# Kernel optimization log

Measured on AMD Instinct MI355X. Metric: run time of the kernel, lower is better.

## Reference

```python
import jax, jax.numpy as jnp
import numpy as np

PARTITION_LENGTH = 64
NUM_PARTITIONS = 1024
BATCH = 2048


def setup_inputs() -> dict:
    key = jax.random.key(0)
    x = jax.random.normal(key, (BATCH, NUM_PARTITIONS * PARTITION_LENGTH), dtype=jnp.float32)
    return {"x": x}


def reference(x) -> jnp.ndarray:
    # Each nn.Linear(partition_length, 1, bias=False) has weight fixed to ones,
    # so it is a sum over a contiguous partition of the feature dim.
    B = x.shape[0]
    # [B, P*L] -> [B, P, L] -> sum over L -> [B, P]
    return x.reshape(B, NUM_PARTITIONS, PARTITION_LENGTH).sum(axis=-1)
```

## Files before the change

### kernel.cpp

```cpp
#include <hip/hip_runtime.h>
#include <hip/hip_bf16.h>


__global__ __launch_bounds__(256) void PartialSum_85478439125876_kernel(
    const float4* __restrict__ x4, float* __restrict__ out, long long n4) {
    long long tid = (long long)blockIdx.x * blockDim.x + threadIdx.x;
    if (tid >= n4) return;

    float4 v = x4[tid];
    float s = v.x + v.y + v.z + v.w;

    s += __shfl_xor(s, 1, 64);
    s += __shfl_xor(s, 2, 64);
    s += __shfl_xor(s, 4, 64);
    s += __shfl_xor(s, 8, 64);

    if ((threadIdx.x & 15) == 0) {
        out[tid >> 4] = s;
    }
}

extern "C" void kernel_launch(void* const* d_in, const int* in_sizes, int n_in,
                              void* d_out, int out_size, void* d_ws, size_t ws_size,
                              hipStream_t stream) {
    const float* x = (const float*)d_in[0];
    float* out = (float*)d_out;

    long long n = (long long)in_sizes[0];
    long long n4 = n / 4;

    const int BLOCK = 256;
    long long grid = (n4 + BLOCK - 1) / BLOCK;

    PartialSum_85478439125876_kernel<<<(unsigned)grid, BLOCK, 0, stream>>>(
        (const float4*)x, out, n4);
}
```

Measured before the change: 651.7 us.

## Stage input via direct global-to-LDS loads and sum partitions per thread

Each block now pulls 64KB of input straight into LDS with global_load_lds 16-byte async loads, then each thread sums one 64-float partition from LDS using swizzled float4 reads. This removes the per-thread cross-lane shuffle reduction and the 1-in-16 output writes, giving coalesced one-output-per-thread stores. In exchange it uses 64KB of LDS per block, which caps occupancy, and the bounds check is gone, so it assumes the input size divides evenly into blocks.

```diff
diff --git a/kernel.cpp b/kernel.cpp
--- a/kernel.cpp
+++ b/kernel.cpp
@@ -1,23 +1,59 @@
 #include <hip/hip_runtime.h>
 #include <hip/hip_bf16.h>
+#include <stdint.h>
 
 
-__global__ __launch_bounds__(256) void PartialSum_85478439125876_kernel(
-    const float4* __restrict__ x4, float* __restrict__ out, long long n4) {
-    long long tid = (long long)blockIdx.x * blockDim.x + threadIdx.x;
-    if (tid >= n4) return;
+#define BLOCK 256
+#define F4_PER_BLOCK 4096
 
-    float4 v = x4[tid];
-    float s = v.x + v.y + v.z + v.w;
+typedef const __attribute__((address_space(1))) uint32_t glb_u32;
+typedef __attribute__((address_space(3))) uint32_t lds_u32;
 
-    s += __shfl_xor(s, 1, 64);
-    s += __shfl_xor(s, 2, 64);
-    s += __shfl_xor(s, 4, 64);
-    s += __shfl_xor(s, 8, 64);
+__global__ __launch_bounds__(BLOCK, 2) void PartialSum_85478439125876_kernel(
+    const float* __restrict__ x, float* __restrict__ out) {
+    __shared__ float4 smem[F4_PER_BLOCK];
 
-    if ((threadIdx.x & 15) == 0) {
-        out[tid >> 4] = s;
+    const int tid = threadIdx.x;
+    const int wave = tid >> 6;
+    const int lane = tid & 63;
+
+    const float* gbase = x + (size_t)blockIdx.x * (F4_PER_BLOCK * 4);
+
+#pragma unroll
+    for (int t = 0; t < 16; ++t) {
+        const int f4 = t * 256 + wave * 64 + lane;
+        glb_u32* g = (glb_u32*)(gbase + (size_t)f4 * 4);
+        lds_u32* l = (lds_u32*)(smem + (t * 256 + wave * 64));
+        __builtin_amdgcn_global_load_lds(g, l, 16, 0, 0);
     }
+
+    __syncthreads();
+
+    const float4* s4 = (const float4*)smem;
+    const int base = tid * 16;
+    const int sw = tid & 7;
+
+    float4 a0 = s4[base + (0 ^ sw)];
+    float4 a1 = s4[base + (1 ^ sw)];
+    float4 a2 = s4[base + (2 ^ sw)];
+    float4 a3 = s4[base + (3 ^ sw)];
+#pragma unroll
+    for (int q = 4; q < 16; q += 4) {
+        float4 v0 = s4[base + ((q + 0) ^ sw)];
+        float4 v1 = s4[base + ((q + 1) ^ sw)];
+        float4 v2 = s4[base + ((q + 2) ^ sw)];
+        float4 v3 = s4[base + ((q + 3) ^ sw)];
+        a0.x += v0.x; a0.y += v0.y; a0.z += v0.z; a0.w += v0.w;
+        a1.x += v1.x; a1.y += v1.y; a1.z += v1.z; a1.w += v1.w;
+        a2.x += v2.x; a2.y += v2.y; a2.z += v2.z; a2.w += v2.w;
+        a3.x += v3.x; a3.y += v3.y; a3.z += v3.z; a3.w += v3.w;
+    }
+    a0.x += a1.x; a0.y += a1.y; a0.z += a1.z; a0.w += a1.w;
+    a2.x += a3.x; a2.y += a3.y; a2.z += a3.z; a2.w += a3.w;
+    a0.x += a2.x; a0.y += a2.y; a0.z += a2.z; a0.w += a2.w;
+    float s = (a0.x + a0.y) + (a0.z + a0.w);
+
+    out[(size_t)blockIdx.x * BLOCK + tid] = s;
 }
 
 extern "C" void kernel_launch(void* const* d_in, const int* in_sizes, int n_in,
@@ -27,11 +63,7 @@
     float* out = (float*)d_out;
 
     long long n = (long long)in_sizes[0];
-    long long n4 = n / 4;
+    long long blocks = n / (F4_PER_BLOCK * 4);
 
-    const int BLOCK = 256;
-    long long grid = (n4 + BLOCK - 1) / BLOCK;
-
-    PartialSum_85478439125876_kernel<<<(unsigned)grid, BLOCK, 0, stream>>>(
-        (const float4*)x, out, n4);
+    PartialSum_85478439125876_kernel<<<(unsigned)blocks, BLOCK, 0, stream>>>(x, out);
 }
```

Result: slower. 672.1 us (+3.1%).
